# Performance work log

Measured on AMD Instinct MI355X. Metric: run time of the kernel, lower is better.

Reference implementation:

```python
import jax, jax.numpy as jnp
import numpy as np

TASKS = 32768          # init kwarg `tasks`
N_HEADS = TASKS + 1    # tasks + 1 distilled/shared head
IN_DIM, HID, OUT = 3, 100, 5


def setup_inputs() -> dict:
    key = jax.random.key(0)
    kx, k1, kb1, k2, kb2 = jax.random.split(key, 5)
    # per-task stacked parameters (equivalent to ModuleList of Linears)
    x = jax.random.normal(kx, (N_HEADS, IN_DIM), dtype=jnp.float32)
    # init scale ~ PyTorch default: U(-1/sqrt(fan_in), 1/sqrt(fan_in)); gaussian approx fine
    W1 = jax.random.normal(k1, (N_HEADS, HID, IN_DIM), dtype=jnp.float32) * (1.0 / np.sqrt(IN_DIM))
    b1 = jax.random.normal(kb1, (N_HEADS, HID), dtype=jnp.float32) * (1.0 / np.sqrt(IN_DIM))
    W2 = jax.random.normal(k2, (N_HEADS, OUT, HID), dtype=jnp.float32) * (1.0 / np.sqrt(HID))
    b2 = jax.random.normal(kb2, (N_HEADS, OUT), dtype=jnp.float32) * (1.0 / np.sqrt(HID))
    return {"x": x, "W1": W1, "b1": b1, "W2": W2, "b2": b2}


def reference(x, W1, b1, W2, b2):
    # x: (T+1, 3) -- one state vector per task head (matches x.view(tasks+1, -1))
    T1 = W1.shape[0]
    x = x.reshape(T1, -1)                                   # (T+1, 3)
    h = jax.nn.relu(jnp.einsum('thi,ti->th', W1, x) + b1)   # (T+1, 100)
    logits = jnp.einsum('toh,th->to', W2, h) + b2           # (T+1, 5)
    return jax.nn.softmax(logits, axis=-1)                  # (T+1, 5)
```

## Files before the change

### kernel.cpp

```cpp
#include <hip/hip_runtime.h>
#include <math.h>


#define N_HEADS 32769
#define HID     100
#define OUT     5

#define WAVES_PER_BLOCK 2
#define NBLOCKS 2816
#define NW      (NBLOCKS * WAVES_PER_BLOCK)

#define RSTRIDE 912
#define OF_B1   300
#define OF_W2   400
#define OF_X    900
#define OF_B2   903

#define GLOBAL_AS __attribute__((address_space(1)))
#define LDS_AS    __attribute__((address_space(3)))

static __device__ __forceinline__ void dma16(const void* g, void* l) {
    __builtin_amdgcn_global_load_lds((const GLOBAL_AS void*)g, (LDS_AS void*)l,
                                     16, 0, 0);
}
static __device__ __forceinline__ void dma4(const void* g, void* l) {
    __builtin_amdgcn_global_load_lds((const GLOBAL_AS void*)g, (LDS_AS void*)l,
                                     4, 0, 0);
}

static __device__ __forceinline__ void stage_head(
    int head, int lane, float* region,
    const float* __restrict__ x,  const float* __restrict__ W1,
    const float* __restrict__ b1, const float* __restrict__ W2,
    const float* __restrict__ b2)
{
    const float* W1h = W1 + (size_t)head * 300;
    const float* b1h = b1 + (size_t)head * 100;
    const float* W2h = W2 + (size_t)head * 500;

    dma16(W1h + 4 * lane,                 region);
    if (lane < 11) dma16(W1h + 256 + 4 * lane, region + 256);
    if (lane < 25) dma16(b1h + 4 * lane,  region + OF_B1);
    dma16(W2h + 4 * lane,                 region + OF_W2);
    if (lane < 61) dma16(W2h + 256 + 4 * lane, region + OF_W2 + 256);
    if (lane < 3)  dma4(x + (size_t)head * 3 + lane, region + OF_X);
    if (lane < 5)  dma4(b2 + (size_t)head * 5 + lane, region + OF_B2);
}

template <int CTRL, int ROW_MASK>
static __device__ __forceinline__ float dpp_add_step(float acc) {
    union { float f; int i; } in, out;
    in.f = acc;
    out.i = __builtin_amdgcn_update_dpp(0, in.i, CTRL, ROW_MASK, 0xF, false);
    return acc + out.f;
}
static __device__ __forceinline__ float wave_reduce_add(float acc) {
    acc = dpp_add_step<0x111, 0xF>(acc);
    acc = dpp_add_step<0x112, 0xF>(acc);
    acc = dpp_add_step<0x114, 0xF>(acc);
    acc = dpp_add_step<0x118, 0xF>(acc);
    acc = dpp_add_step<0x142, 0xA>(acc);
    acc = dpp_add_step<0x143, 0xC>(acc);
    union { float f; int i; } v, r;
    v.f = acc;
    r.i = __builtin_amdgcn_readlane(v.i, 63);
    return r.f;
}

__global__ __launch_bounds__(128) void distral_kernel(
    const float* __restrict__ x,
    const float* __restrict__ W1,
    const float* __restrict__ b1,
    const float* __restrict__ W2,
    const float* __restrict__ b2,
    float* __restrict__ out)
{
    __shared__ float lds[WAVES_PER_BLOCK][2][RSTRIDE];

    const int lane = threadIdx.x & 63;
    const int wv   = threadIdx.x >> 6;
    const int w    = blockIdx.x * WAVES_PER_BLOCK + wv;

    int head = w;
    stage_head(head, lane, &lds[wv][0][0], x, W1, b1, W2, b2);

    int buf = 0;
    for (;;) {
        const int  nh   = head + NW;
        const bool more = (nh < N_HEADS);
        const int  lh   = more ? nh : w;
        stage_head(lh, lane, &lds[wv][buf ^ 1][0], x, W1, b1, W2, b2);

        asm volatile("" ::: "memory");
        __builtin_amdgcn_s_waitcnt(0x0F77);
        asm volatile("" ::: "memory");

        const float* region = &lds[wv][buf][0];

        const float x0 = region[OF_X + 0];
        const float x1 = region[OF_X + 1];
        const float x2 = region[OF_X + 2];

        const bool has2 = (lane < HID - 64);
        const int  j2   = has2 ? (lane + 64) : (HID - 1);

        float h0, h1;
        {
            const float* r = region + 3 * lane;
            h0 = fmaxf(fmaf(r[0], x0, fmaf(r[1], x1, fmaf(r[2], x2,
                       region[OF_B1 + lane]))), 0.0f);
        }
        {
            const float* r = region + 3 * j2;
            h1 = fmaxf(fmaf(r[0], x0, fmaf(r[1], x1, fmaf(r[2], x2,
                       region[OF_B1 + j2]))), 0.0f);
            h1 = has2 ? h1 : 0.0f;
        }

        float logit[OUT];
#pragma unroll
        for (int o = 0; o < OUT; ++o) {
            float p = fmaf(region[OF_W2 + o * HID + j2], h1,
                           region[OF_W2 + o * HID + lane] * h0);
            logit[o] = wave_reduce_add(p) + region[OF_B2 + o];
        }

        float m = -INFINITY;
#pragma unroll
        for (int o = 0; o < OUT; ++o) m = fmaxf(m, logit[o]);
        float e[OUT], s = 0.0f;
#pragma unroll
        for (int o = 0; o < OUT; ++o) { e[o] = __expf(logit[o] - m); s += e[o]; }
        const float inv = 1.0f / s;

        if (lane < OUT) {
            float v = (lane == 0) ? e[0]
                    : (lane == 1) ? e[1]
                    : (lane == 2) ? e[2]
                    : (lane == 3) ? e[3]
                    :               e[4];
            out[(size_t)head * OUT + lane] = v * inv;
        }

        if (!more) break;
        head = nh;
        buf ^= 1;
    }
}

extern "C" void kernel_launch(void* const* d_in, const int* in_sizes, int n_in,
                              void* d_out, int out_size, void* d_ws, size_t ws_size,
                              hipStream_t stream) {
    const float* x  = (const float*)d_in[0];
    const float* W1 = (const float*)d_in[1];
    const float* b1 = (const float*)d_in[2];
    const float* W2 = (const float*)d_in[3];
    const float* b2 = (const float*)d_in[4];
    float* out = (float*)d_out;

    distral_kernel<<<NBLOCKS, 128, 0, stream>>>(x, W1, b1, W2, b2, out);
}
```

Baseline: 146.9 us.

## Replace persistent double-buffered loop with fixed two-heads-per-wave grid

Drops the persistent grid-stride loop (2816 blocks) and launches enough blocks that each wave stages exactly two heads into LDS up front, then computes them one after another using partial vmcnt waits. x and b2 are now read through scalar/global loads instead of being DMA'd into LDS. The aim is to expose more memory parallelism across many short-lived waves and remove per-iteration loop overhead. The cost is launching around 8k blocks with no cross-iteration prefetch, so latency hiding now depends entirely on occupancy.

```diff
diff --git a/kernel.cpp b/kernel.cpp
--- a/kernel.cpp
+++ b/kernel.cpp
@@ -7,14 +7,9 @@
 #define OUT     5
 
 #define WAVES_PER_BLOCK 2
-#define NBLOCKS 2816
-#define NW      (NBLOCKS * WAVES_PER_BLOCK)
-
-#define RSTRIDE 912
-#define OF_B1   300
-#define OF_W2   400
-#define OF_X    900
-#define OF_B2   903
+#define HEAD_F 900
+#define OF_B1  300
+#define OF_W2  400
 
 #define GLOBAL_AS __attribute__((address_space(1)))
 #define LDS_AS    __attribute__((address_space(3)))
@@ -23,28 +18,21 @@
     __builtin_amdgcn_global_load_lds((const GLOBAL_AS void*)g, (LDS_AS void*)l,
                                      16, 0, 0);
 }
-static __device__ __forceinline__ void dma4(const void* g, void* l) {
-    __builtin_amdgcn_global_load_lds((const GLOBAL_AS void*)g, (LDS_AS void*)l,
-                                     4, 0, 0);
-}
 
 static __device__ __forceinline__ void stage_head(
     int head, int lane, float* region,
-    const float* __restrict__ x,  const float* __restrict__ W1,
-    const float* __restrict__ b1, const float* __restrict__ W2,
-    const float* __restrict__ b2)
+    const float* __restrict__ W1, const float* __restrict__ b1,
+    const float* __restrict__ W2)
 {
     const float* W1h = W1 + (size_t)head * 300;
     const float* b1h = b1 + (size_t)head * 100;
     const float* W2h = W2 + (size_t)head * 500;
 
-    dma16(W1h + 4 * lane,                 region);
+    dma16(W1h + 4 * lane,                      region);
     if (lane < 11) dma16(W1h + 256 + 4 * lane, region + 256);
-    if (lane < 25) dma16(b1h + 4 * lane,  region + OF_B1);
-    dma16(W2h + 4 * lane,                 region + OF_W2);
+    if (lane < 25) dma16(b1h + 4 * lane,       region + OF_B1);
+    dma16(W2h + 4 * lane,                      region + OF_W2);
     if (lane < 61) dma16(W2h + 256 + 4 * lane, region + OF_W2 + 256);
-    if (lane < 3)  dma4(x + (size_t)head * 3 + lane, region + OF_X);
-    if (lane < 5)  dma4(b2 + (size_t)head * 5 + lane, region + OF_B2);
 }
 
 template <int CTRL, int ROW_MASK>
@@ -67,6 +55,58 @@
     return r.f;
 }
 
+static __device__ __forceinline__ void compute_head(
+    const float* region, int head, int lane, bool do_store,
+    const float* __restrict__ x, const float* __restrict__ b2,
+    float* __restrict__ out)
+{
+    const int sh = __builtin_amdgcn_readfirstlane(head);
+    const float x0 = x[sh * 3 + 0];
+    const float x1 = x[sh * 3 + 1];
+    const float x2 = x[sh * 3 + 2];
+
+    const bool has2 = (lane < HID - 64);
+    const int  j2   = has2 ? (lane + 64) : (HID - 1);
+
+    float h0, h1;
+    {
+        const float* r = region + 3 * lane;
+        h0 = fmaxf(fmaf(r[0], x0, fmaf(r[1], x1, fmaf(r[2], x2,
+                   region[OF_B1 + lane]))), 0.0f);
+    }
+    {
+        const float* r = region + 3 * j2;
+        h1 = fmaxf(fmaf(r[0], x0, fmaf(r[1], x1, fmaf(r[2], x2,
+                   region[OF_B1 + j2]))), 0.0f);
+        h1 = has2 ? h1 : 0.0f;
+    }
+
+    float logit[OUT];
+#pragma unroll
+    for (int o = 0; o < OUT; ++o) {
+        float p = fmaf(region[OF_W2 + o * HID + j2], h1,
+                       region[OF_W2 + o * HID + lane] * h0);
+        logit[o] = wave_reduce_add(p) + b2[sh * OUT + o];
+    }
+
+    float m = -INFINITY;
+#pragma unroll
+    for (int o = 0; o < OUT; ++o) m = fmaxf(m, logit[o]);
+    float e[OUT], s = 0.0f;
+#pragma unroll
+    for (int o = 0; o < OUT; ++o) { e[o] = __expf(logit[o] - m); s += e[o]; }
+    const float inv = 1.0f / s;
+
+    if (do_store && lane < OUT) {
+        float v = (lane == 0) ? e[0]
+                : (lane == 1) ? e[1]
+                : (lane == 2) ? e[2]
+                : (lane == 3) ? e[3]
+                :               e[4];
+        out[(size_t)head * OUT + lane] = v * inv;
+    }
+}
+
 __global__ __launch_bounds__(128) void distral_kernel(
     const float* __restrict__ x,
     const float* __restrict__ W1,
@@ -75,77 +115,29 @@
     const float* __restrict__ b2,
     float* __restrict__ out)
 {
-    __shared__ float lds[WAVES_PER_BLOCK][2][RSTRIDE];
+    __shared__ float lds[WAVES_PER_BLOCK][2][HEAD_F];
 
     const int lane = threadIdx.x & 63;
     const int wv   = threadIdx.x >> 6;
-    const int w    = blockIdx.x * WAVES_PER_BLOCK + wv;
 
-    int head = w;
-    stage_head(head, lane, &lds[wv][0][0], x, W1, b1, W2, b2);
+    const int base   = blockIdx.x * (2 * WAVES_PER_BLOCK) + 2 * wv;
+    const bool v0    = (base     < N_HEADS);
+    const bool v1    = (base + 1 < N_HEADS);
+    const int headA  = v0 ? base     : 0;
+    const int headB  = v1 ? base + 1 : headA;
 
-    int buf = 0;
-    for (;;) {
-        const int  nh   = head + NW;
-        const bool more = (nh < N_HEADS);
-        const int  lh   = more ? nh : w;
-        stage_head(lh, lane, &lds[wv][buf ^ 1][0], x, W1, b1, W2, b2);
+    stage_head(headA, lane, &lds[wv][0][0], W1, b1, W2);
+    stage_head(headB, lane, &lds[wv][1][0], W1, b1, W2);
 
-        asm volatile("" ::: "memory");
-        __builtin_amdgcn_s_waitcnt(0x0F77);
-        asm volatile("" ::: "memory");
+    asm volatile("" ::: "memory");
+    __builtin_amdgcn_s_waitcnt(0x0F75);
+    asm volatile("" ::: "memory");
+    compute_head(&lds[wv][0][0], headA, lane, v0, x, b2, out);
 
-        const float* region = &lds[wv][buf][0];
-
-        const float x0 = region[OF_X + 0];
-        const float x1 = region[OF_X + 1];
-        const float x2 = region[OF_X + 2];
-
-        const bool has2 = (lane < HID - 64);
-        const int  j2   = has2 ? (lane + 64) : (HID - 1);
-
-        float h0, h1;
-        {
-            const float* r = region + 3 * lane;
-            h0 = fmaxf(fmaf(r[0], x0, fmaf(r[1], x1, fmaf(r[2], x2,
-                       region[OF_B1 + lane]))), 0.0f);
-        }
-        {
-            const float* r = region + 3 * j2;
-            h1 = fmaxf(fmaf(r[0], x0, fmaf(r[1], x1, fmaf(r[2], x2,
-                       region[OF_B1 + j2]))), 0.0f);
-            h1 = has2 ? h1 : 0.0f;
-        }
-
-        float logit[OUT];
-#pragma unroll
-        for (int o = 0; o < OUT; ++o) {
-            float p = fmaf(region[OF_W2 + o * HID + j2], h1,
-                           region[OF_W2 + o * HID + lane] * h0);
-            logit[o] = wave_reduce_add(p) + region[OF_B2 + o];
-        }
-
-        float m = -INFINITY;
-#pragma unroll
-        for (int o = 0; o < OUT; ++o) m = fmaxf(m, logit[o]);
-        float e[OUT], s = 0.0f;
-#pragma unroll
-        for (int o = 0; o < OUT; ++o) { e[o] = __expf(logit[o] - m); s += e[o]; }
-        const float inv = 1.0f / s;
-
-        if (lane < OUT) {
-            float v = (lane == 0) ? e[0]
-                    : (lane == 1) ? e[1]
-                    : (lane == 2) ? e[2]
-                    : (lane == 3) ? e[3]
-                    :               e[4];
-            out[(size_t)head * OUT + lane] = v * inv;
-        }
-
-        if (!more) break;
-        head = nh;
-        buf ^= 1;
-    }
+    asm volatile("" ::: "memory");
+    __builtin_amdgcn_s_waitcnt(0x0F71);
+    asm volatile("" ::: "memory");
+    compute_head(&lds[wv][1][0], headB, lane, v1, x, b2, out);
 }
 
 extern "C" void kernel_launch(void* const* d_in, const int* in_sizes, int n_in,
@@ -158,5 +150,7 @@
     const float* b2 = (const float*)d_in[4];
     float* out = (float*)d_out;
 
-    distral_kernel<<<NBLOCKS, 128, 0, stream>>>(x, W1, b1, W2, b2, out);
+    const int heads_per_block = 2 * WAVES_PER_BLOCK;
+    const int blocks = (N_HEADS + heads_per_block - 1) / heads_per_block;
+    distral_kernel<<<blocks, 128, 0, stream>>>(x, W1, b1, W2, b2, out);
 }
```

New measurement: 142.7 us. 1.03x faster.
